# Kernel tuning notes

Measured on AMD Instinct MI355X. Metric: run time of the kernel, lower is better.

Reference implementation:

```python
import jax, jax.numpy as jnp
import numpy as np
from jax import lax

V_TH = 1.0    # init kwarg 'thresh'
ALPHA = 1.0   # init kwarg 'alpha' (surrogate-gradient width, unused in fwd)

T, B, N = 32, 32, 65536


def setup_inputs() -> dict:
    key = jax.random.key(0)
    x = jax.random.normal(key, (T, B, N), dtype=jnp.float32)
    return {"x": x}


def reference(x) -> jnp.ndarray:
    # Integrate-and-fire neuron, TBN layout, sequential scan over time:
    #   m_t = v_{t-1} + x_t            (integrate)
    #   y_t = heaviside(m_t - v_th)    (fire)
    #   v_t = m_t - y_t * v_th         (soft reset by subtraction)
    def step(v, x_t):
        m = v + x_t
        y = (m >= V_TH).astype(x_t.dtype)
        v_new = m - y * V_TH
        return v_new, y

    v0 = jnp.zeros_like(x[0])
    _, y_seq = lax.scan(step, v0, x)
    return y_seq
```

## Files before the change

kernel.cpp:

```cpp
#include <hip/hip_runtime.h>


typedef float v4f __attribute__((ext_vector_type(4)));

#define T_STEPS 32
#define PF 8

__global__ __launch_bounds__(256, 8) void if_kernel(const v4f* __restrict__ x,
                                                    v4f* __restrict__ y,
                                                    int bn4) {
    int idx = blockIdx.x * blockDim.x + threadIdx.x;
    if (idx >= bn4) return;

    const v4f* xp = x + idx;
    v4f* yp = y + idx;

    v4f buf[PF];
#pragma unroll
    for (int i = 0; i < PF; ++i)
        buf[i] = xp[(size_t)i * bn4];

    v4f v = (v4f){0.f, 0.f, 0.f, 0.f};

#pragma unroll
    for (int t = 0; t < T_STEPS; ++t) {
        v4f xv = buf[t % PF];
        if (t + PF < T_STEPS)
            buf[t % PF] = xp[(size_t)(t + PF) * bn4];

        v4f m = v + xv;
        v4f out;
        out.x = (m.x >= 1.0f) ? 1.0f : 0.0f;
        out.y = (m.y >= 1.0f) ? 1.0f : 0.0f;
        out.z = (m.z >= 1.0f) ? 1.0f : 0.0f;
        out.w = (m.w >= 1.0f) ? 1.0f : 0.0f;
        v = m - out;

        __builtin_nontemporal_store(out, yp + (size_t)t * bn4);
    }
}

extern "C" void kernel_launch(void* const* d_in, const int* in_sizes, int n_in,
                              void* d_out, int out_size, void* d_ws, size_t ws_size,
                              hipStream_t stream) {
    const float* x = (const float*)d_in[0];
    float* y = (float*)d_out;

    int total = in_sizes[0];
    int bn = total / T_STEPS;
    int bn4 = bn / 4;

    int block = 256;
    int grid = (bn4 + block - 1) / block;

    if_kernel<<<grid, block, 0, stream>>>((const v4f*)x, (v4f*)y, bn4);
}
```

Before: 486.5 us.

## Split IF scan into load-all compute phase and bitmask-driven store phase

Replaces the 8-deep rolling prefetch buffer with a fully unrolled loop that issues all 32 time-step loads up front, packs spike bits into per-lane 32-bit masks, then writes all outputs in a second loop. The goal is to let the compiler hoist every load for maximum memory-level parallelism and separate read and write traffic phases. It also changes the reset to a select instead of a subtraction of the spike value. The risk is higher register pressure (32 v4f loads in flight) under launch_bounds(256,8), which could cause spills or lower occupancy.

New measurement: 458.1 us. 5.8% less time.

```diff
diff --git a/kernel.cpp b/kernel.cpp
--- a/kernel.cpp
+++ b/kernel.cpp
@@ -4,7 +4,6 @@
 typedef float v4f __attribute__((ext_vector_type(4)));
 
 #define T_STEPS 32
-#define PF 8
 
 __global__ __launch_bounds__(256, 8) void if_kernel(const v4f* __restrict__ x,
                                                     v4f* __restrict__ y,
@@ -13,29 +12,39 @@
     if (idx >= bn4) return;
 
     const v4f* xp = x + idx;
-    v4f* yp = y + idx;
 
-    v4f buf[PF];
-#pragma unroll
-    for (int i = 0; i < PF; ++i)
-        buf[i] = xp[(size_t)i * bn4];
-
-    v4f v = (v4f){0.f, 0.f, 0.f, 0.f};
+    float v0 = 0.f, v1 = 0.f, v2 = 0.f, v3 = 0.f;
+    unsigned m0 = 0u, m1 = 0u, m2 = 0u, m3 = 0u;
 
 #pragma unroll
     for (int t = 0; t < T_STEPS; ++t) {
-        v4f xv = buf[t % PF];
-        if (t + PF < T_STEPS)
-            buf[t % PF] = xp[(size_t)(t + PF) * bn4];
+        v4f xv = xp[(size_t)t * bn4];
+        float a0 = v0 + xv.x;
+        float a1 = v1 + xv.y;
+        float a2 = v2 + xv.z;
+        float a3 = v3 + xv.w;
+        bool s0 = a0 >= 1.0f;
+        bool s1 = a1 >= 1.0f;
+        bool s2 = a2 >= 1.0f;
+        bool s3 = a3 >= 1.0f;
+        m0 |= (unsigned)s0 << t;
+        m1 |= (unsigned)s1 << t;
+        m2 |= (unsigned)s2 << t;
+        m3 |= (unsigned)s3 << t;
+        v0 = s0 ? a0 - 1.0f : a0;
+        v1 = s1 ? a1 - 1.0f : a1;
+        v2 = s2 ? a2 - 1.0f : a2;
+        v3 = s3 ? a3 - 1.0f : a3;
+    }
 
-        v4f m = v + xv;
+    v4f* yp = y + idx;
+#pragma unroll
+    for (int t = 0; t < T_STEPS; ++t) {
         v4f out;
-        out.x = (m.x >= 1.0f) ? 1.0f : 0.0f;
-        out.y = (m.y >= 1.0f) ? 1.0f : 0.0f;
-        out.z = (m.z >= 1.0f) ? 1.0f : 0.0f;
-        out.w = (m.w >= 1.0f) ? 1.0f : 0.0f;
-        v = m - out;
-
+        out.x = ((m0 >> t) & 1u) ? 1.0f : 0.0f;
+        out.y = ((m1 >> t) & 1u) ? 1.0f : 0.0f;
+        out.z = ((m2 >> t) & 1u) ? 1.0f : 0.0f;
+        out.w = ((m3 >> t) & 1u) ? 1.0f : 0.0f;
         __builtin_nontemporal_store(out, yp + (size_t)t * bn4);
     }
 }
```
